# Kernel optimization log

Measured on AMD Instinct MI355X. Metric: run time of the kernel, lower is better.

## Reference

```python
import jax, jax.numpy as jnp
import numpy as np

B, D = 65536, 512
EPS = 1e-15
MAXN = 1.0 - 4e-3  # geoopt fp32 ball boundary, c = 1


def _norm(x):
    return jnp.sqrt(jnp.clip(jnp.sum(x * x, -1, keepdims=True), EPS))


def _artanh(x):
    return jnp.arctanh(jnp.clip(x, -1.0 + 1e-7, 1.0 - 1e-7))


def projx(x):
    n = _norm(x)
    return jnp.where(n > MAXN, x / n * MAXN, x)


def mobius_add(x, y):
    x2 = jnp.sum(x * x, -1, keepdims=True)
    y2 = jnp.sum(y * y, -1, keepdims=True)
    xy = jnp.sum(x * y, -1, keepdims=True)
    num = (1.0 + 2.0 * xy + y2) * x + (1.0 - x2) * y
    den = 1.0 + 2.0 * xy + x2 * y2
    return num / jnp.maximum(den, EPS)


def expmap(x, u):
    un = _norm(u)
    lam = 2.0 / jnp.maximum(1.0 - jnp.sum(x * x, -1, keepdims=True), EPS)
    return mobius_add(x, jnp.tanh(lam * un / 2.0) * u / un)


def logmap(x, y):
    sub = mobius_add(-x, y)
    sn = _norm(sub)
    lam = 2.0 / jnp.maximum(1.0 - jnp.sum(x * x, -1, keepdims=True), EPS)
    return (2.0 / lam) * _artanh(sn) * sub / sn


def expmap0(u):
    un = _norm(u)
    return jnp.tanh(un) * u / un


def logmap0(y):
    yn = _norm(y)
    return _artanh(yn) * y / yn


def mobius_scalar_mul(r, x):
    xn = _norm(x)
    return jnp.tanh(r * _artanh(xn)) * x / xn


def poincare_fc(x, z, bias):
    # HNN++ Poincare fully-connected layer, c = 1
    zn = jnp.sqrt(jnp.clip(jnp.sum(z * z, 0), EPS))   # [out]
    z_unit = z / zn                                   # [in, out]
    two_r = 2.0 * bias                                # [out]
    cx2 = jnp.sum(x * x, -1, keepdims=True)           # [B, 1]
    inner = x @ z_unit                                # [B, out]
    v = 2.0 * zn * jnp.arcsinh(
        (2.0 * inner * jnp.cosh(two_r) - (1.0 + cx2) * jnp.sinh(two_r))
        / jnp.maximum(1.0 - cx2, EPS))
    w = jnp.sinh(v)
    return w / (1.0 + jnp.sqrt(1.0 + jnp.sum(w * w, -1, keepdims=True)))


def setup_inputs():
    key = jax.random.key(0)
    k1, k2, k3 = jax.random.split(key, 3)
    u1 = jax.random.normal(k1, (B, D), jnp.float32)
    u2 = jax.random.normal(k2, (B, D), jnp.float32)
    # points strictly inside the unit Poincare ball
    x_current = 0.7 * u1 / (1.0 + _norm(u1))
    x_previous = 0.7 * u2 / (1.0 + _norm(u2))
    # PoincareLinear id_init: 0.5*I, plus tiny noise so grads/outputs are non-degenerate
    z = 0.5 * jnp.eye(D, dtype=jnp.float32) + 0.01 * jax.random.normal(k3, (D, D), jnp.float32)
    bias = jnp.zeros((D,), jnp.float32)
    alpha = jnp.asarray(0.7, jnp.float32)
    step_size = jnp.asarray(1.0, jnp.float32)
    return {"x_current": x_current, "x_previous": x_previous, "z": z,
            "bias": bias, "alpha": alpha, "step_size": step_size}


def reference(x_current, x_previous, z, bias, alpha, step_size):
    # backward trajectory via logmap on the manifold (x_previous given)
    bt = logmap(x_previous, x_current)
    step = jax.nn.sigmoid(step_size)
    # PoincareLinear: expmap0 -> poincare_fc -> logmap0
    vel = logmap0(poincare_fc(expmap0(bt), z, bias))
    x_update = projx(expmap(x_current, step * vel))
    a = jax.nn.sigmoid(alpha)
    # poincare_residual_update
    xc = projx(x_current)
    xu = projx(x_update)
    x_next = projx(mobius_add(mobius_scalar_mul(a, xc), mobius_scalar_mul(1.0 - a, xu)))
    return (x_next, xc)
```

## Files before the change

### kernel.cpp

```cpp
#include <hip/hip_runtime.h>
#include <stdint.h>

#define DDIM 512
#define BROWS 65536
#define EPSF 1e-15f
#define MAXNF 0.996f
#define SQRT_EPSF 3.1622776e-8f
#define ATANH_CLIP 0.99999988f

typedef __bf16 bf16x8 __attribute__((ext_vector_type(8)));
typedef float f32x4 __attribute__((ext_vector_type(4)));

__device__ __forceinline__ unsigned short f2bf(float f) {
    union { float f; uint32_t u; } c; c.f = f;
    uint32_t u = c.u;
    u += 0x7fffu + ((u >> 16) & 1u);
    return (unsigned short)(u >> 16);
}

__device__ __forceinline__ float rcpf(float x) { return __builtin_amdgcn_rcpf(x); }

__device__ __forceinline__ float wred(float v) {
    v += __shfl_xor(v, 1);
    v += __shfl_xor(v, 2);
    v += __shfl_xor(v, 4);
    v += __shfl_xor(v, 8);
    v += __shfl_xor(v, 16);
    v += __shfl_xor(v, 32);
    return v;
}

__device__ __forceinline__ float fast_tanh_pos(float x) {
    float t = __expf(-2.0f * x);
    return (1.0f - t) * rcpf(1.0f + t);
}
__device__ __forceinline__ float fast_atanh_pos(float x) {
    return 0.5f * __logf((1.0f + x) * rcpf(1.0f - x));
}
__device__ __forceinline__ float fast_asinh(float t) {
    float a = fabsf(t);
    float r = __logf(a + sqrtf(fmaf(a, a, 1.0f)));
    return copysignf(r, t);
}
__device__ __forceinline__ float fast_sinh(float v) {
    float q = __expf(v);
    return 0.5f * (q - rcpf(q));
}

__global__ void prep_kernel(const float* __restrict__ z, const float* __restrict__ bias,
                            float* __restrict__ znf, float* __restrict__ chv,
                            float* __restrict__ shv, unsigned short* __restrict__ zT) {
    int j = blockIdx.x;
    int l = threadIdx.x;
    float zv[8];
    float s = 0.f;
#pragma unroll
    for (int t = 0; t < 8; ++t) {
        float v = z[(size_t)(t * 64 + l) * DDIM + j];
        zv[t] = v;
        s = fmaf(v, v, s);
    }
    s = wred(s);
    float zn = sqrtf(fmaxf(s, EPSF));
    float inv = 1.0f / zn;
#pragma unroll
    for (int t = 0; t < 8; ++t)
        zT[(size_t)j * DDIM + t * 64 + l] = f2bf(zv[t] * inv);
    if (l == 0) {
        znf[j] = zn;
        float tr = 2.0f * bias[j];
        chv[j] = coshf(tr);
        shv[j] = sinhf(tr);
    }
}

__global__ __launch_bounds__(512, 4) void hpd_main(
    const float* __restrict__ Xc, const float* __restrict__ Xp,
    const float* __restrict__ znf, const float* __restrict__ chv, const float* __restrict__ shv,
    const unsigned short* __restrict__ zT,
    const float* __restrict__ alpha_p, const float* __restrict__ step_p,
    float* __restrict__ out)
{
    __shared__ __align__(16) unsigned char smem[70656];
    float* cx2s = (float*)(smem + 65536);
    float* dccs = (float*)(smem + 65792);
    float* swp  = (float*)(smem + 66048);
    float* cwp  = (float*)(smem + 68096);
    float* ans  = (float*)(smem + 70144);
    float* bns  = (float*)(smem + 70400);

    const int t = threadIdx.x;
    const int w = t >> 6;
    const int l = t & 63;
    const int l15 = l & 15;
    const int quad = l >> 4;
    const int r0 = blockIdx.x * 64;

    float a_sig = rcpf(1.0f + __expf(-alpha_p[0]));
    float step_sig = rcpf(1.0f + __expf(-step_p[0]));

    float* out1 = out + (size_t)BROWS * DDIM;

#pragma unroll
    for (int idx = 0; idx < 8; ++idx) {
        int row = w * 4 + (idx & 3) + ((idx >> 2) << 5);
        const float* pc = Xc + (size_t)(r0 + row) * DDIM + l * 8;
        const float* pp = Xp + (size_t)(r0 + row) * DDIM + l * 8;
        float4 c0 = *(const float4*)pc; float4 c1 = *(const float4*)(pc + 4);
        float4 p0 = *(const float4*)pp; float4 p1 = *(const float4*)(pp + 4);
        float xcv[8] = {c0.x, c0.y, c0.z, c0.w, c1.x, c1.y, c1.z, c1.w};
        float xpv[8] = {p0.x, p0.y, p0.z, p0.w, p1.x, p1.y, p1.z, p1.w};
        float dcc = 0.f, dpp = 0.f, dpc = 0.f;
#pragma unroll
        for (int j = 0; j < 8; ++j) {
            dcc = fmaf(xcv[j], xcv[j], dcc);
            dpp = fmaf(xpv[j], xpv[j], dpp);
            dpc = fmaf(xpv[j], xcv[j], dpc);
        }
        dcc = wred(dcc); dpp = wred(dpp); dpc = wred(dpc);
        float Ca = -(1.0f - 2.0f * dpc + dcc);
        float Cb = 1.0f - dpp;
        float den = fmaxf(1.0f - 2.0f * dpc + dpp * dcc, EPSF);
        float rden = rcpf(den);
        float ssub = (Ca * Ca * dpp + 2.0f * Ca * Cb * dpc + Cb * Cb * dcc) * rden * rden;
        float sn = sqrtf(fmaxf(ssub, EPSF));
        float tol = fmaxf(1.0f - dpp, EPSF);
        float art = fast_atanh_pos(fminf(sn, ATANH_CLIP));
        float sbt = tol * art * rcpf(sn);
        float un = fmaxf(tol * art, SQRT_EPSF);
        float te = fast_tanh_pos(un);
        float se = te * rcpf(un) * sbt;
        float cep = se * Ca * rden;
        float cex = se * Cb * rden;
        if (l == 0) { cx2s[row] = te * te; dccs[row] = dcc; }
        float nx = sqrtf(fmaxf(dcc, EPSF));
        float sxc = (nx > MAXNF) ? (MAXNF * rcpf(nx)) : 1.0f;
        float* po1 = out1 + (size_t)(r0 + row) * DDIM + l * 8;
        *(float4*)po1 = make_float4(sxc * xcv[0], sxc * xcv[1], sxc * xcv[2], sxc * xcv[3]);
        *(float4*)(po1 + 4) = make_float4(sxc * xcv[4], sxc * xcv[5], sxc * xcv[6], sxc * xcv[7]);
        unsigned short e8[8];
#pragma unroll
        for (int j = 0; j < 8; ++j)
            e8[j] = f2bf(fmaf(cex, xcv[j], cep * xpv[j]));
        uint32_t u0 = (uint32_t)e8[0] | ((uint32_t)e8[1] << 16);
        uint32_t u1 = (uint32_t)e8[2] | ((uint32_t)e8[3] << 16);
        uint32_t u2 = (uint32_t)e8[4] | ((uint32_t)e8[5] << 16);
        uint32_t u3 = (uint32_t)e8[6] | ((uint32_t)e8[7] << 16);
        uint32_t off = row * 1024 + ((l ^ (row & 7)) * 16);
        *(uint4*)(smem + off) = make_uint4(u0, u1, u2, u3);
    }
    __syncthreads();

    f32x4 acc[4][4];
#pragma unroll
    for (int m = 0; m < 4; ++m)
#pragma unroll
        for (int j = 0; j < 4; ++j)
            acc[m][j] = (f32x4){0.f, 0.f, 0.f, 0.f};

    const unsigned short* zbase = zT + (size_t)(w * 64 + l15) * DDIM + quad * 8;
#pragma unroll 1
    for (int ks = 0; ks < 16; ++ks) {
        bf16x8 af[4], bfr[4];
#pragma unroll
        for (int j = 0; j < 4; ++j)
            bfr[j] = *(const bf16x8*)(zbase + (size_t)j * 16 * DDIM + ks * 32);
#pragma unroll
        for (int m = 0; m < 4; ++m) {
            int row = m * 16 + l15;
            af[m] = *(const bf16x8*)(smem + row * 1024 + (((ks * 4 + quad) ^ (row & 7)) * 16));
        }
#pragma unroll
        for (int m = 0; m < 4; ++m)
#pragma unroll
            for (int j = 0; j < 4; ++j)
                acc[m][j] = __builtin_amdgcn_mfma_f32_16x16x32_bf16(af[m], bfr[j], acc[m][j], 0, 0, 0);
    }

    float znv[4], chc[4], shc[4];
#pragma unroll
    for (int j = 0; j < 4; ++j) {
        int col = w * 64 + j * 16 + l15;
        znv[j] = znf[col]; chc[j] = chv[col]; shc[j] = shv[col];
    }
    const float* xb = Xc + (size_t)r0 * DDIM + w * 64 + l15;

#pragma unroll
    for (int m = 0; m < 4; ++m) {
        int rbase = m * 16 + quad * 4;
        float inv1m[4], opc[4];
#pragma unroll
        for (int r = 0; r < 4; ++r) {
            float c2 = cx2s[rbase + r];
            inv1m[r] = rcpf(fmaxf(1.0f - c2, EPSF));
            opc[r] = 1.0f + c2;
        }
        float swr[4] = {0.f, 0.f, 0.f, 0.f}, cwr[4] = {0.f, 0.f, 0.f, 0.f};
#pragma unroll
        for (int j = 0; j < 4; ++j) {
#pragma unroll
            for (int r = 0; r < 4; ++r) {
                float inner = acc[m][j][r];
                float arg = fmaf(2.0f * inner, chc[j], -opc[r] * shc[j]) * inv1m[r];
                float v = 2.0f * znv[j] * fast_asinh(arg);
                float wv = fast_sinh(v);
                acc[m][j][r] = wv;
                float xv = xb[(size_t)(rbase + r) * DDIM + j * 16];
                swr[r] = fmaf(wv, wv, swr[r]);
                cwr[r] = fmaf(xv, wv, cwr[r]);
            }
        }
#pragma unroll
        for (int r = 0; r < 4; ++r) {
            float s = swr[r], c = cwr[r];
            s += __shfl_xor(s, 1); s += __shfl_xor(s, 2); s += __shfl_xor(s, 4); s += __shfl_xor(s, 8);
            c += __shfl_xor(c, 1); c += __shfl_xor(c, 2); c += __shfl_xor(c, 4); c += __shfl_xor(c, 8);
            if (l15 == 0) { swp[(rbase + r) * 8 + w] = s; cwp[(rbase + r) * 8 + w] = c; }
        }
    }
    __syncthreads();

    if (t < 64) {
        int row = t;
        float4 s0 = *(const float4*)(swp + row * 8);
        float4 s1 = *(const float4*)(swp + row * 8 + 4);
        float sw = ((s0.x + s0.y) + (s0.z + s0.w)) + ((s1.x + s1.y) + (s1.z + s1.w));
        float4 q0 = *(const float4*)(cwp + row * 8);
        float4 q1 = *(const float4*)(cwp + row * 8 + 4);
        float cw = ((q0.x + q0.y) + (q0.z + q0.w)) + ((q1.x + q1.y) + (q1.z + q1.w));
        float dcc = dccs[row];
        float is = 1.0f / (1.0f + sqrtf(1.0f + sw));
        float nfc = sqrtf(fmaxf(sw * is * is, EPSF));
        float artf = fast_atanh_pos(fminf(nfc, ATANH_CLIP));
        float un2 = fmaxf(step_sig * artf, SQRT_EPSF);
        float g = fast_tanh_pos(un2 / fmaxf(1.0f - dcc, EPSF));
        float by = g * is / nfc;
        float xy = by * cw;
        float y2 = by * by * sw;
        float P = 1.0f + 2.0f * xy + y2;
        float den2 = fmaxf(1.0f + 2.0f * xy + dcc * y2, EPSF);
        float a1 = P / den2;
        float b1 = (1.0f - dcc) * by / den2;
        float s2u = a1 * a1 * dcc + 2.0f * a1 * b1 * cw + b1 * b1 * sw;
        float nxu = sqrtf(fmaxf(s2u, EPSF));
        float pj = (nxu > MAXNF) ? (MAXNF / nxu) : 1.0f;
        a1 *= pj; b1 *= pj;
        float nxu2 = fminf(nxu, MAXNF);
        float nx = sqrtf(fmaxf(dcc, EPSF));
        float sxc = (nx > MAXNF) ? (MAXNF / nx) : 1.0f;
        float nxc = fminf(nx, MAXNF);
        float A1 = fast_tanh_pos(a_sig * fast_atanh_pos(fminf(nxc, ATANH_CLIP))) / nxc * sxc;
        float t2s = fast_tanh_pos((1.0f - a_sig) * fast_atanh_pos(fminf(nxu2, ATANH_CLIP)));
        float sm2 = t2s / fmaxf(nxu2, SQRT_EPSF);
        float A2 = sm2 * a1, B2 = sm2 * b1;
        float x2m = A1 * A1 * dcc;
        float y2m = A2 * A2 * dcc + 2.0f * A2 * B2 * cw + B2 * B2 * sw;
        float xym = A1 * (A2 * dcc + B2 * cw);
        float num1 = 1.0f + 2.0f * xym + y2m;
        float num2 = 1.0f - x2m;
        float den3 = fmaxf(1.0f + 2.0f * xym + x2m * y2m, EPSF);
        float an = (num1 * A1 + num2 * A2) / den3;
        float bn = (num2 * B2) / den3;
        float s2n = an * an * dcc + 2.0f * an * bn * cw + bn * bn * sw;
        float nn = sqrtf(fmaxf(s2n, EPSF));
        float pj2 = (nn > MAXNF) ? (MAXNF / nn) : 1.0f;
        ans[row] = an * pj2;
        bns[row] = bn * pj2;
    }
    __syncthreads();

    float* ob = out + (size_t)r0 * DDIM + w * 64 + l15;
#pragma unroll
    for (int m = 0; m < 4; ++m) {
        int rbase = m * 16 + quad * 4;
        float anv[4], bnv[4];
#pragma unroll
        for (int r = 0; r < 4; ++r) { anv[r] = ans[rbase + r]; bnv[r] = bns[rbase + r]; }
#pragma unroll
        for (int j = 0; j < 4; ++j) {
#pragma unroll
            for (int r = 0; r < 4; ++r) {
                float xv = xb[(size_t)(rbase + r) * DDIM + j * 16];
                ob[(size_t)(rbase + r) * DDIM + j * 16] = fmaf(anv[r], xv, bnv[r] * acc[m][j][r]);
            }
        }
    }
}

extern "C" void kernel_launch(void* const* d_in, const int* in_sizes, int n_in,
                              void* d_out, int out_size, void* d_ws, size_t ws_size,
                              hipStream_t stream) {
    const float* xc = (const float*)d_in[0];
    const float* xp = (const float*)d_in[1];
    const float* z = (const float*)d_in[2];
    const float* bias = (const float*)d_in[3];
    const float* alpha = (const float*)d_in[4];
    const float* stepsz = (const float*)d_in[5];
    float* out = (float*)d_out;

    float* znf = (float*)d_ws;
    float* chv = znf + 512;
    float* shv = znf + 1024;
    unsigned short* zT = (unsigned short*)(znf + 1536);

    prep_kernel<<<512, 64, 0, stream>>>(z, bias, znf, chv, shv, zT);
    hpd_main<<<BROWS / 64, 512, 0, stream>>>(xc, xp, znf, chv, shv, zT, alpha, stepsz, out);
}
```

Before: 569.1 us.

## Batch row loads and reductions, double-buffer Z fragments, hoist epilogue loads

The prologue now loads four rows at once and interleaves their butterfly reductions, which raises memory-level and shuffle-level parallelism. The MFMA k-loop is fully unrolled and the Z fragments are double-buffered, so each global load is issued one step ahead of its use. In both epilogues the Xc loads are hoisted into a register block ahead of the arithmetic. Register pressure rises, which may lower occupancy.

Result: no change. 563.1 us (-1.1%).

```diff
diff --git a/kernel.cpp b/kernel.cpp
--- a/kernel.cpp
+++ b/kernel.cpp
@@ -102,52 +102,73 @@
     float* out1 = out + (size_t)BROWS * DDIM;
 
 #pragma unroll
-    for (int idx = 0; idx < 8; ++idx) {
-        int row = w * 4 + (idx & 3) + ((idx >> 2) << 5);
-        const float* pc = Xc + (size_t)(r0 + row) * DDIM + l * 8;
-        const float* pp = Xp + (size_t)(r0 + row) * DDIM + l * 8;
-        float4 c0 = *(const float4*)pc; float4 c1 = *(const float4*)(pc + 4);
-        float4 p0 = *(const float4*)pp; float4 p1 = *(const float4*)(pp + 4);
-        float xcv[8] = {c0.x, c0.y, c0.z, c0.w, c1.x, c1.y, c1.z, c1.w};
-        float xpv[8] = {p0.x, p0.y, p0.z, p0.w, p1.x, p1.y, p1.z, p1.w};
-        float dcc = 0.f, dpp = 0.f, dpc = 0.f;
-#pragma unroll
-        for (int j = 0; j < 8; ++j) {
-            dcc = fmaf(xcv[j], xcv[j], dcc);
-            dpp = fmaf(xpv[j], xpv[j], dpp);
-            dpc = fmaf(xpv[j], xcv[j], dpc);
-        }
-        dcc = wred(dcc); dpp = wred(dpp); dpc = wred(dpc);
-        float Ca = -(1.0f - 2.0f * dpc + dcc);
-        float Cb = 1.0f - dpp;
-        float den = fmaxf(1.0f - 2.0f * dpc + dpp * dcc, EPSF);
-        float rden = rcpf(den);
-        float ssub = (Ca * Ca * dpp + 2.0f * Ca * Cb * dpc + Cb * Cb * dcc) * rden * rden;
-        float sn = sqrtf(fmaxf(ssub, EPSF));
-        float tol = fmaxf(1.0f - dpp, EPSF);
-        float art = fast_atanh_pos(fminf(sn, ATANH_CLIP));
-        float sbt = tol * art * rcpf(sn);
-        float un = fmaxf(tol * art, SQRT_EPSF);
-        float te = fast_tanh_pos(un);
-        float se = te * rcpf(un) * sbt;
-        float cep = se * Ca * rden;
-        float cex = se * Cb * rden;
-        if (l == 0) { cx2s[row] = te * te; dccs[row] = dcc; }
-        float nx = sqrtf(fmaxf(dcc, EPSF));
-        float sxc = (nx > MAXNF) ? (MAXNF * rcpf(nx)) : 1.0f;
-        float* po1 = out1 + (size_t)(r0 + row) * DDIM + l * 8;
-        *(float4*)po1 = make_float4(sxc * xcv[0], sxc * xcv[1], sxc * xcv[2], sxc * xcv[3]);
-        *(float4*)(po1 + 4) = make_float4(sxc * xcv[4], sxc * xcv[5], sxc * xcv[6], sxc * xcv[7]);
-        unsigned short e8[8];
-#pragma unroll
-        for (int j = 0; j < 8; ++j)
-            e8[j] = f2bf(fmaf(cex, xcv[j], cep * xpv[j]));
-        uint32_t u0 = (uint32_t)e8[0] | ((uint32_t)e8[1] << 16);
-        uint32_t u1 = (uint32_t)e8[2] | ((uint32_t)e8[3] << 16);
-        uint32_t u2 = (uint32_t)e8[4] | ((uint32_t)e8[5] << 16);
-        uint32_t u3 = (uint32_t)e8[6] | ((uint32_t)e8[7] << 16);
-        uint32_t off = row * 1024 + ((l ^ (row & 7)) * 16);
-        *(uint4*)(smem + off) = make_uint4(u0, u1, u2, u3);
+    for (int g = 0; g < 2; ++g) {
+        const int rowb = w * 4 + (g << 5);
+        float xcv[4][8], xpv[4][8];
+#pragma unroll
+        for (int q = 0; q < 4; ++q) {
+            const float* pc = Xc + (size_t)(r0 + rowb + q) * DDIM + l * 8;
+            const float* pp = Xp + (size_t)(r0 + rowb + q) * DDIM + l * 8;
+            *(float4*)&xcv[q][0] = *(const float4*)pc;
+            *(float4*)&xcv[q][4] = *(const float4*)(pc + 4);
+            *(float4*)&xpv[q][0] = *(const float4*)pp;
+            *(float4*)&xpv[q][4] = *(const float4*)(pp + 4);
+        }
+        float dcc[4], dpp[4], dpc[4];
+#pragma unroll
+        for (int q = 0; q < 4; ++q) {
+            float a = 0.f, b = 0.f, c = 0.f;
+#pragma unroll
+            for (int j = 0; j < 8; ++j) {
+                a = fmaf(xcv[q][j], xcv[q][j], a);
+                b = fmaf(xpv[q][j], xpv[q][j], b);
+                c = fmaf(xpv[q][j], xcv[q][j], c);
+            }
+            dcc[q] = a; dpp[q] = b; dpc[q] = c;
+        }
+#pragma unroll
+        for (int s = 1; s < 64; s <<= 1) {
+#pragma unroll
+            for (int q = 0; q < 4; ++q) {
+                dcc[q] += __shfl_xor(dcc[q], s);
+                dpp[q] += __shfl_xor(dpp[q], s);
+                dpc[q] += __shfl_xor(dpc[q], s);
+            }
+        }
+#pragma unroll
+        for (int q = 0; q < 4; ++q) {
+            const int row = rowb + q;
+            float Ca = -(1.0f - 2.0f * dpc[q] + dcc[q]);
+            float Cb = 1.0f - dpp[q];
+            float den = fmaxf(1.0f - 2.0f * dpc[q] + dpp[q] * dcc[q], EPSF);
+            float rden = rcpf(den);
+            float ssub = (Ca * Ca * dpp[q] + 2.0f * Ca * Cb * dpc[q] + Cb * Cb * dcc[q]) * rden * rden;
+            float sn = sqrtf(fmaxf(ssub, EPSF));
+            float tol = fmaxf(1.0f - dpp[q], EPSF);
+            float art = fast_atanh_pos(fminf(sn, ATANH_CLIP));
+            float sbt = tol * art * rcpf(sn);
+            float un = fmaxf(tol * art, SQRT_EPSF);
+            float te = fast_tanh_pos(un);
+            float se = te * rcpf(un) * sbt;
+            float cep = se * Ca * rden;
+            float cex = se * Cb * rden;
+            if (l == 0) { cx2s[row] = te * te; dccs[row] = dcc[q]; }
+            float nx = sqrtf(fmaxf(dcc[q], EPSF));
+            float sxc = (nx > MAXNF) ? (MAXNF * rcpf(nx)) : 1.0f;
+            float* po1 = out1 + (size_t)(r0 + row) * DDIM + l * 8;
+            *(float4*)po1 = make_float4(sxc * xcv[q][0], sxc * xcv[q][1], sxc * xcv[q][2], sxc * xcv[q][3]);
+            *(float4*)(po1 + 4) = make_float4(sxc * xcv[q][4], sxc * xcv[q][5], sxc * xcv[q][6], sxc * xcv[q][7]);
+            unsigned short e8[8];
+#pragma unroll
+            for (int j = 0; j < 8; ++j)
+                e8[j] = f2bf(fmaf(cex, xcv[q][j], cep * xpv[q][j]));
+            uint32_t u0 = (uint32_t)e8[0] | ((uint32_t)e8[1] << 16);
+            uint32_t u1 = (uint32_t)e8[2] | ((uint32_t)e8[3] << 16);
+            uint32_t u2 = (uint32_t)e8[4] | ((uint32_t)e8[5] << 16);
+            uint32_t u3 = (uint32_t)e8[6] | ((uint32_t)e8[7] << 16);
+            uint32_t off = row * 1024 + ((l ^ (row & 7)) * 16);
+            *(uint4*)(smem + off) = make_uint4(u0, u1, u2, u3);
+        }
     }
     __syncthreads();
 
@@ -159,12 +180,19 @@
             acc[m][j] = (f32x4){0.f, 0.f, 0.f, 0.f};
 
     const unsigned short* zbase = zT + (size_t)(w * 64 + l15) * DDIM + quad * 8;
-#pragma unroll 1
+    bf16x8 bbuf[2][4];
+#pragma unroll
+    for (int j = 0; j < 4; ++j)
+        bbuf[0][j] = *(const bf16x8*)(zbase + (size_t)j * 16 * DDIM);
+#pragma unroll
     for (int ks = 0; ks < 16; ++ks) {
-        bf16x8 af[4], bfr[4];
-#pragma unroll
-        for (int j = 0; j < 4; ++j)
-            bfr[j] = *(const bf16x8*)(zbase + (size_t)j * 16 * DDIM + ks * 32);
+        const int cur = ks & 1;
+        if (ks < 15) {
+#pragma unroll
+            for (int j = 0; j < 4; ++j)
+                bbuf[cur ^ 1][j] = *(const bf16x8*)(zbase + (size_t)j * 16 * DDIM + (ks + 1) * 32);
+        }
+        bf16x8 af[4];
 #pragma unroll
         for (int m = 0; m < 4; ++m) {
             int row = m * 16 + l15;
@@ -174,7 +202,7 @@
         for (int m = 0; m < 4; ++m)
 #pragma unroll
             for (int j = 0; j < 4; ++j)
-                acc[m][j] = __builtin_amdgcn_mfma_f32_16x16x32_bf16(af[m], bfr[j], acc[m][j], 0, 0, 0);
+                acc[m][j] = __builtin_amdgcn_mfma_f32_16x16x32_bf16(af[m], bbuf[cur][j], acc[m][j], 0, 0, 0);
     }
 
     float znv[4], chc[4], shc[4];
@@ -188,6 +216,12 @@
 #pragma unroll
     for (int m = 0; m < 4; ++m) {
         int rbase = m * 16 + quad * 4;
+        float xv[4][4];
+#pragma unroll
+        for (int j = 0; j < 4; ++j)
+#pragma unroll
+            for (int r = 0; r < 4; ++r)
+                xv[j][r] = xb[(size_t)(rbase + r) * DDIM + j * 16];
         float inv1m[4], opc[4];
 #pragma unroll
         for (int r = 0; r < 4; ++r) {
@@ -205,9 +239,8 @@
                 float v = 2.0f * znv[j] * fast_asinh(arg);
                 float wv = fast_sinh(v);
                 acc[m][j][r] = wv;
-                float xv = xb[(size_t)(rbase + r) * DDIM + j * 16];
                 swr[r] = fmaf(wv, wv, swr[r]);
-                cwr[r] = fmaf(xv, wv, cwr[r]);
+                cwr[r] = fmaf(xv[j][r], wv, cwr[r]);
             }
         }
 #pragma unroll
@@ -273,16 +306,20 @@
 #pragma unroll
     for (int m = 0; m < 4; ++m) {
         int rbase = m * 16 + quad * 4;
+        float xv[4][4];
+#pragma unroll
+        for (int j = 0; j < 4; ++j)
+#pragma unroll
+            for (int r = 0; r < 4; ++r)
+                xv[j][r] = xb[(size_t)(rbase + r) * DDIM + j * 16];
         float anv[4], bnv[4];
 #pragma unroll
         for (int r = 0; r < 4; ++r) { anv[r] = ans[rbase + r]; bnv[r] = bns[rbase + r]; }
 #pragma unroll
         for (int j = 0; j < 4; ++j) {
 #pragma unroll
-            for (int r = 0; r < 4; ++r) {
-                float xv = xb[(size_t)(rbase + r) * DDIM + j * 16];
-                ob[(size_t)(rbase + r) * DDIM + j * 16] = fmaf(anv[r], xv, bnv[r] * acc[m][j][r]);
-            }
+            for (int r = 0; r < 4; ++r)
+                ob[(size_t)(rbase + r) * DDIM + j * 16] = fmaf(anv[r], xv[j][r], bnv[r] * acc[m][j][r]);
         }
     }
 }
```

## Stream input rows via async global-to-LDS loads with smaller 32-row blocks

Applied to the files above, without the earlier changes.

Row inputs Xc and Xp are now fetched with global_load_lds into double-buffered per-wave LDS slots. Each row's load is issued two rows ahead, and explicit vmcnt waits let the load latency overlap with the per-row hyperbolic math. Blocks shrink to 32 rows and 256 threads, so each wave covers 128 output columns with a 2x8 MFMA tile. The x-value loads in the epilogue are hoisted into register arrays. The changes trade register pressure and the hand-written waitcnt counting, which is fragile, for better latency hiding and higher occupancy per CU.

Result: slower. 581.3 us (+2.1%).

```diff
diff --git a/kernel.cpp b/kernel.cpp
--- a/kernel.cpp
+++ b/kernel.cpp
@@ -47,6 +47,12 @@
     return 0.5f * (q - rcpf(q));
 }
 
+__device__ __forceinline__ void glds16(const float* g, unsigned char* lds) {
+    __builtin_amdgcn_global_load_lds(
+        (const __attribute__((address_space(1))) void*)g,
+        (__attribute__((address_space(3))) void*)lds, 16, 0, 0);
+}
+
 __global__ void prep_kernel(const float* __restrict__ z, const float* __restrict__ bias,
                             float* __restrict__ znf, float* __restrict__ chv,
                             float* __restrict__ shv, unsigned short* __restrict__ zT) {
@@ -74,120 +80,156 @@
     }
 }
 
-__global__ __launch_bounds__(512, 4) void hpd_main(
+
+#define ISSUE_ROW(k)                                                          \
+  {                                                                           \
+    const int irow_ = (w << 3) + (k);                                         \
+    unsigned char* isb_ = smem + 32768 + (w << 13) + (((k) & 1) << 12);       \
+    const float* irc_ = Xc + (size_t)(r0 + irow_) * DDIM + l * 4;             \
+    const float* irp_ = Xp + (size_t)(r0 + irow_) * DDIM + l * 4;             \
+    glds16(irc_, isb_);                                                       \
+    glds16(irc_ + 256, isb_ + 1024);                                          \
+    glds16(irp_, isb_ + 2048);                                                \
+    glds16(irp_ + 256, isb_ + 3072);                                          \
+  }
+
+#define PROC_ROW(k, WNSTR)                                                    \
+  {                                                                           \
+    const int row_ = (w << 3) + (k);                                          \
+    unsigned char* sb_ = smem + 32768 + (w << 13) + (((k) & 1) << 12);        \
+    asm volatile("s_waitcnt vmcnt(" WNSTR ")" ::: "memory");                  \
+    float4 cA = *(const float4*)(sb_ + l * 16);                               \
+    float4 cB = *(const float4*)(sb_ + 1024 + l * 16);                        \
+    float4 pA = *(const float4*)(sb_ + 2048 + l * 16);                        \
+    float4 pB = *(const float4*)(sb_ + 3072 + l * 16);                        \
+    float c8[8] = {cA.x, cA.y, cA.z, cA.w, cB.x, cB.y, cB.z, cB.w};           \
+    float p8[8] = {pA.x, pA.y, pA.z, pA.w, pB.x, pB.y, pB.z, pB.w};           \
+    float dcc = 0.f, dpp = 0.f, dpc = 0.f;                                    \
+    _Pragma("unroll") for (int j_ = 0; j_ < 8; ++j_) {                        \
+      dcc = fmaf(c8[j_], c8[j_], dcc);                                        \
+      dpp = fmaf(p8[j_], p8[j_], dpp);                                        \
+      dpc = fmaf(p8[j_], c8[j_], dpc);                                        \
+    }                                                                         \
+    _Pragma("unroll") for (int s_ = 1; s_ < 64; s_ <<= 1) {                   \
+      dcc += __shfl_xor(dcc, s_);                                             \
+      dpp += __shfl_xor(dpp, s_);                                             \
+      dpc += __shfl_xor(dpc, s_);                                             \
+    }                                                                         \
+    __builtin_amdgcn_sched_barrier(0);                                        \
+    if ((k) < 6) ISSUE_ROW((k) + 2);                                          \
+    __builtin_amdgcn_sched_barrier(0);                                        \
+    float Ca = -(1.0f - 2.0f * dpc + dcc);                                    \
+    float Cb = 1.0f - dpp;                                                    \
+    float den = fmaxf(1.0f - 2.0f * dpc + dpp * dcc, EPSF);                   \
+    float rden = rcpf(den);                                                   \
+    float ssub = (Ca * Ca * dpp + 2.0f * Ca * Cb * dpc + Cb * Cb * dcc) * rden * rden; \
+    float sn = sqrtf(fmaxf(ssub, EPSF));                                      \
+    float tol = fmaxf(1.0f - dpp, EPSF);                                      \
+    float art = fast_atanh_pos(fminf(sn, ATANH_CLIP));                        \
+    float sbt = tol * art * rcpf(sn);                                         \
+    float un = fmaxf(tol * art, SQRT_EPSF);                                   \
+    float te = fast_tanh_pos(un);                                             \
+    float se = te * rcpf(un) * sbt;                                           \
+    float cep = se * Ca * rden;                                               \
+    float cex = se * Cb * rden;                                               \
+    if (l == 0) { cx2s[row_] = te * te; dccs[row_] = dcc; }                   \
+    float nx = sqrtf(fmaxf(dcc, EPSF));                                       \
+    float sxc = (nx > MAXNF) ? (MAXNF * rcpf(nx)) : 1.0f;                     \
+    float* po1 = out1 + (size_t)(r0 + row_) * DDIM + l * 4;                   \
+    unsigned short e8[8];                                                     \
+    _Pragma("unroll") for (int j_ = 0; j_ < 8; ++j_)                          \
+      e8[j_] = f2bf(fmaf(cex, c8[j_], cep * p8[j_]));                         \
+    uint32_t offA_ = row_ * 1024 + ((((l >> 1) ^ (row_ & 7)) << 4) | ((l & 1) << 3)); \
+    uint32_t offB_ = row_ * 1024 + (((((l >> 1) + 32) ^ (row_ & 7)) << 4) | ((l & 1) << 3)); \
+    *(uint2*)(smem + offA_) = make_uint2((uint32_t)e8[0] | ((uint32_t)e8[1] << 16), \
+                                         (uint32_t)e8[2] | ((uint32_t)e8[3] << 16)); \
+    *(uint2*)(smem + offB_) = make_uint2((uint32_t)e8[4] | ((uint32_t)e8[5] << 16), \
+                                         (uint32_t)e8[6] | ((uint32_t)e8[7] << 16)); \
+    *(float4*)po1 = make_float4(sxc * c8[0], sxc * c8[1], sxc * c8[2], sxc * c8[3]); \
+    *(float4*)(po1 + 256) = make_float4(sxc * c8[4], sxc * c8[5], sxc * c8[6], sxc * c8[7]); \
+  }
+
+__global__ __launch_bounds__(256, 2) void hpd_main(
     const float* __restrict__ Xc, const float* __restrict__ Xp,
     const float* __restrict__ znf, const float* __restrict__ chv, const float* __restrict__ shv,
     const unsigned short* __restrict__ zT,
     const float* __restrict__ alpha_p, const float* __restrict__ step_p,
     float* __restrict__ out)
 {
-    __shared__ __align__(16) unsigned char smem[70656];
+    __shared__ __align__(16) unsigned char smem[65792];
+    float* swp  = (float*)(smem + 32768);
+    float* cwp  = (float*)(smem + 33280);
+    float* ans  = (float*)(smem + 33792);
+    float* bns  = (float*)(smem + 33920);
     float* cx2s = (float*)(smem + 65536);
-    float* dccs = (float*)(smem + 65792);
-    float* swp  = (float*)(smem + 66048);
-    float* cwp  = (float*)(smem + 68096);
-    float* ans  = (float*)(smem + 70144);
-    float* bns  = (float*)(smem + 70400);
+    float* dccs = (float*)(smem + 65664);
 
     const int t = threadIdx.x;
     const int w = t >> 6;
     const int l = t & 63;
     const int l15 = l & 15;
     const int quad = l >> 4;
-    const int r0 = blockIdx.x * 64;
+    const int r0 = blockIdx.x * 32;
 
     float a_sig = rcpf(1.0f + __expf(-alpha_p[0]));
     float step_sig = rcpf(1.0f + __expf(-step_p[0]));
-
     float* out1 = out + (size_t)BROWS * DDIM;
 
-#pragma unroll
-    for (int idx = 0; idx < 8; ++idx) {
-        int row = w * 4 + (idx & 3) + ((idx >> 2) << 5);
-        const float* pc = Xc + (size_t)(r0 + row) * DDIM + l * 8;
-        const float* pp = Xp + (size_t)(r0 + row) * DDIM + l * 8;
-        float4 c0 = *(const float4*)pc; float4 c1 = *(const float4*)(pc + 4);
-        float4 p0 = *(const float4*)pp; float4 p1 = *(const float4*)(pp + 4);
-        float xcv[8] = {c0.x, c0.y, c0.z, c0.w, c1.x, c1.y, c1.z, c1.w};
-        float xpv[8] = {p0.x, p0.y, p0.z, p0.w, p1.x, p1.y, p1.z, p1.w};
-        float dcc = 0.f, dpp = 0.f, dpc = 0.f;
-#pragma unroll
-        for (int j = 0; j < 8; ++j) {
-            dcc = fmaf(xcv[j], xcv[j], dcc);
-            dpp = fmaf(xpv[j], xpv[j], dpp);
-            dpc = fmaf(xpv[j], xcv[j], dpc);
-        }
-        dcc = wred(dcc); dpp = wred(dpp); dpc = wred(dpc);
-        float Ca = -(1.0f - 2.0f * dpc + dcc);
-        float Cb = 1.0f - dpp;
-        float den = fmaxf(1.0f - 2.0f * dpc + dpp * dcc, EPSF);
-        float rden = rcpf(den);
-        float ssub = (Ca * Ca * dpp + 2.0f * Ca * Cb * dpc + Cb * Cb * dcc) * rden * rden;
-        float sn = sqrtf(fmaxf(ssub, EPSF));
-        float tol = fmaxf(1.0f - dpp, EPSF);
-        float art = fast_atanh_pos(fminf(sn, ATANH_CLIP));
-        float sbt = tol * art * rcpf(sn);
-        float un = fmaxf(tol * art, SQRT_EPSF);
-        float te = fast_tanh_pos(un);
-        float se = te * rcpf(un) * sbt;
-        float cep = se * Ca * rden;
-        float cex = se * Cb * rden;
-        if (l == 0) { cx2s[row] = te * te; dccs[row] = dcc; }
-        float nx = sqrtf(fmaxf(dcc, EPSF));
-        float sxc = (nx > MAXNF) ? (MAXNF * rcpf(nx)) : 1.0f;
-        float* po1 = out1 + (size_t)(r0 + row) * DDIM + l * 8;
-        *(float4*)po1 = make_float4(sxc * xcv[0], sxc * xcv[1], sxc * xcv[2], sxc * xcv[3]);
-        *(float4*)(po1 + 4) = make_float4(sxc * xcv[4], sxc * xcv[5], sxc * xcv[6], sxc * xcv[7]);
-        unsigned short e8[8];
+    ISSUE_ROW(0); ISSUE_ROW(1);
+    PROC_ROW(0, "4");
+    PROC_ROW(1, "6");
+    PROC_ROW(2, "8");
+    PROC_ROW(3, "8");
+    PROC_ROW(4, "8");
+    PROC_ROW(5, "8");
+    PROC_ROW(6, "8");
+    PROC_ROW(7, "4");
+    __syncthreads();
+
+    f32x4 acc[2][8];
+#pragma unroll
+    for (int m = 0; m < 2; ++m)
 #pragma unroll
         for (int j = 0; j < 8; ++j)
-            e8[j] = f2bf(fmaf(cex, xcv[j], cep * xpv[j]));
-        uint32_t u0 = (uint32_t)e8[0] | ((uint32_t)e8[1] << 16);
-        uint32_t u1 = (uint32_t)e8[2] | ((uint32_t)e8[3] << 16);
-        uint32_t u2 = (uint32_t)e8[4] | ((uint32_t)e8[5] << 16);
-        uint32_t u3 = (uint32_t)e8[6] | ((uint32_t)e8[7] << 16);
-        uint32_t off = row * 1024 + ((l ^ (row & 7)) * 16);
-        *(uint4*)(smem + off) = make_uint4(u0, u1, u2, u3);
-    }
-    __syncthreads();
-
-    f32x4 acc[4][4];
-#pragma unroll
-    for (int m = 0; m < 4; ++m)
-#pragma unroll
-        for (int j = 0; j < 4; ++j)
             acc[m][j] = (f32x4){0.f, 0.f, 0.f, 0.f};
 
-    const unsigned short* zbase = zT + (size_t)(w * 64 + l15) * DDIM + quad * 8;
-#pragma unroll 1
+    const unsigned short* zbase = zT + (size_t)(w * 128 + l15) * DDIM + quad * 8;
+#pragma unroll
     for (int ks = 0; ks < 16; ++ks) {
-        bf16x8 af[4], bfr[4];
-#pragma unroll
-        for (int j = 0; j < 4; ++j)
+        bf16x8 bfr[8];
+#pragma unroll
+        for (int j = 0; j < 8; ++j)
             bfr[j] = *(const bf16x8*)(zbase + (size_t)j * 16 * DDIM + ks * 32);
-#pragma unroll
-        for (int m = 0; m < 4; ++m) {
+        bf16x8 af[2];
+#pragma unroll
+        for (int m = 0; m < 2; ++m) {
             int row = m * 16 + l15;
             af[m] = *(const bf16x8*)(smem + row * 1024 + (((ks * 4 + quad) ^ (row & 7)) * 16));
         }
 #pragma unroll
-        for (int m = 0; m < 4; ++m)
-#pragma unroll
-            for (int j = 0; j < 4; ++j)
+        for (int m = 0; m < 2; ++m)
+#pragma unroll
+            for (int j = 0; j < 8; ++j)
                 acc[m][j] = __builtin_amdgcn_mfma_f32_16x16x32_bf16(af[m], bfr[j], acc[m][j], 0, 0, 0);
     }
 
-    float znv[4], chc[4], shc[4];
-#pragma unroll
-    for (int j = 0; j < 4; ++j) {
-        int col = w * 64 + j * 16 + l15;
+    float znv[8], chc[8], shc[8];
+#pragma unroll
+    for (int j = 0; j < 8; ++j) {
+        int col = w * 128 + j * 16 + l15;
         znv[j] = znf[col]; chc[j] = chv[col]; shc[j] = shv[col];
     }
-    const float* xb = Xc + (size_t)r0 * DDIM + w * 64 + l15;
-
-#pragma unroll
-    for (int m = 0; m < 4; ++m) {
+    const float* xb = Xc + (size_t)r0 * DDIM + w * 128 + l15;
+
+#pragma unroll
+    for (int m = 0; m < 2; ++m) {
         int rbase = m * 16 + quad * 4;
+        float xv[8][4];
+#pragma unroll
+        for (int j = 0; j < 8; ++j)
+#pragma unroll
+            for (int r = 0; r < 4; ++r)
+                xv[j][r] = xb[(size_t)(rbase + r) * DDIM + j * 16];
         float inv1m[4], opc[4];
 #pragma unroll
         for (int r = 0; r < 4; ++r) {
@@ -197,7 +239,7 @@
         }
         float swr[4] = {0.f, 0.f, 0.f, 0.f}, cwr[4] = {0.f, 0.f, 0.f, 0.f};
 #pragma unroll
-        for (int j = 0; j < 4; ++j) {
+        for (int j = 0; j < 8; ++j) {
 #pragma unroll
             for (int r = 0; r < 4; ++r) {
                 float inner = acc[m][j][r];
@@ -205,9 +247,8 @@
                 float v = 2.0f * znv[j] * fast_asinh(arg);
                 float wv = fast_sinh(v);
                 acc[m][j][r] = wv;
-                float xv = xb[(size_t)(rbase + r) * DDIM + j * 16];
                 swr[r] = fmaf(wv, wv, swr[r]);
-                cwr[r] = fmaf(xv, wv, cwr[r]);
+                cwr[r] = fmaf(xv[j][r], wv, cwr[r]);
             }
         }
 #pragma unroll
@@ -215,19 +256,17 @@
             float s = swr[r], c = cwr[r];
             s += __shfl_xor(s, 1); s += __shfl_xor(s, 2); s += __shfl_xor(s, 4); s += __shfl_xor(s, 8);
             c += __shfl_xor(c, 1); c += __shfl_xor(c, 2); c += __shfl_xor(c, 4); c += __shfl_xor(c, 8);
-            if (l15 == 0) { swp[(rbase + r) * 8 + w] = s; cwp[(rbase + r) * 8 + w] = c; }
+            if (l15 == 0) { swp[(rbase + r) * 4 + w] = s; cwp[(rbase + r) * 4 + w] = c; }
         }
     }
     __syncthreads();
 
-    if (t < 64) {
+    if (t < 32) {
         int row = t;
-        float4 s0 = *(const float4*)(swp + row * 8);
-        float4 s1 = *(const float4*)(swp + row * 8 + 4);
-        float sw = ((s0.x + s0.y) + (s0.z + s0.w)) + ((s1.x + s1.y) + (s1.z + s1.w));
-        float4 q0 = *(const float4*)(cwp + row * 8);
-        float4 q1 = *(const float4*)(cwp + row * 8 + 4);
-        float cw = ((q0.x + q0.y) + (q0.z + q0.w)) + ((q1.x + q1.y) + (q1.z + q1.w));
+        float4 s0 = *(const float4*)(swp + row * 4);
+        float sw = (s0.x + s0.y) + (s0.z + s0.w);
+        float4 q0 = *(const float4*)(cwp + row * 4);
+        float cw = (q0.x + q0.y) + (q0.z + q0.w);
         float dcc = dccs[row];
         float is = 1.0f / (1.0f + sqrtf(1.0f + sw));
         float nfc = sqrtf(fmaxf(sw * is * is, EPSF));
@@ -269,20 +308,24 @@
     }
     __syncthreads();
 
-    float* ob = out + (size_t)r0 * DDIM + w * 64 + l15;
-#pragma unroll
-    for (int m = 0; m < 4; ++m) {
+    float* ob = out + (size_t)r0 * DDIM + w * 128 + l15;
+#pragma unroll
+    for (int m = 0; m < 2; ++m) {
         int rbase = m * 16 + quad * 4;
+        float xv[8][4];
+#pragma unroll
+        for (int j = 0; j < 8; ++j)
+#pragma unroll
+            for (int r = 0; r < 4; ++r)
+                xv[j][r] = xb[(size_t)(rbase + r) * DDIM + j * 16];
         float anv[4], bnv[4];
 #pragma unroll
         for (int r = 0; r < 4; ++r) { anv[r] = ans[rbase + r]; bnv[r] = bns[rbase + r]; }
 #pragma unroll
-        for (int j = 0; j < 4; ++j) {
-#pragma unroll
-            for (int r = 0; r < 4; ++r) {
-                float xv = xb[(size_t)(rbase + r) * DDIM + j * 16];
-                ob[(size_t)(rbase + r) * DDIM + j * 16] = fmaf(anv[r], xv, bnv[r] * acc[m][j][r]);
-            }
+        for (int j = 0; j < 8; ++j) {
+#pragma unroll
+            for (int r = 0; r < 4; ++r)
+                ob[(size_t)(rbase + r) * DDIM + j * 16] = fmaf(anv[r], xv[j][r], bnv[r] * acc[m][j][r]);
         }
     }
 }
@@ -304,5 +347,5 @@
     unsigned short* zT = (unsigned short*)(znf + 1536);
 
     prep_kernel<<<512, 64, 0, stream>>>(z, bias, znf, chv, shv, zT);
-    hpd_main<<<BROWS / 64, 512, 0, stream>>>(xc, xp, znf, chv, shv, zT, alpha, stepsz, out);
-}
+    hpd_main<<<BROWS / 32, 256, 0, stream>>>(xc, xp, znf, chv, shv, zT, alpha, stepsz, out);
+}
```
